# Kernel tuning notes

Measured on AMD Instinct MI355X. Metric: run time of the kernel, lower is better.

Reference implementation:

```python
import jax, jax.numpy as jnp
import numpy as np

B, N, NV = 2, 4096, 32768
HID = 128
XD, YD, ZD = 128, 128, 16  # dense occupancy grid dims (original derives from coord maxima)


def setup_inputs() -> dict:
    key = jax.random.key(0)
    ks = jax.random.split(key, 12)
    position = jax.random.normal(ks[0], (B, N, 3), jnp.float32) * 20.0
    scale = jax.random.uniform(ks[1], (B, N, 3), jnp.float32)
    rotation = jax.random.normal(ks[2], (B, N, 4), jnp.float32)
    opacity = jax.random.uniform(ks[3], (B, N, 1), jnp.float32)
    # sparse voxel coords: [batch_idx, x, y, z]
    b_idx = jax.random.randint(ks[4], (NV, 1), 0, B)
    xs = jax.random.randint(ks[5], (NV, 1), 0, XD)
    ys = jax.random.randint(ks[6], (NV, 1), 0, YD)
    zs = jax.random.randint(ks[7], (NV, 1), 0, ZD)
    voxel_coords = jnp.concatenate([b_idx, xs, ys, zs], axis=1).astype(jnp.int32)
    # MLP params: Linear(11,128) -> ReLU -> Linear(128,128)
    W1 = jax.random.normal(ks[8], (11, HID), jnp.float32) * (1.0 / np.sqrt(11))
    b1 = jnp.zeros((HID,), jnp.float32)
    W2 = jax.random.normal(ks[9], (HID, HID), jnp.float32) * (1.0 / np.sqrt(HID))
    b2 = jnp.zeros((HID,), jnp.float32)
    return {"position": position, "scale": scale, "rotation": rotation,
            "opacity": opacity, "W1": W1, "b1": b1, "W2": W2, "b2": b2,
            "voxel_coords": voxel_coords}


def reference(position, scale, rotation, opacity, W1, b1, W2, b2, voxel_coords):
    # concat gaussian attributes -> (B, N, 11)
    x = jnp.concatenate([position, scale, rotation, opacity], axis=-1)
    x = jnp.maximum(x @ W1 + b1, 0.0) @ W2 + b2  # (B, N, HID)

    # anchor grid: linspace(-50,50, N^(1/3))^3 -> (N, 3)
    n_side = int(round(N ** (1.0 / 3.0)))
    anchor_pos = jnp.linspace(-50.0, 50.0, n_side)
    grid = jnp.stack(jnp.meshgrid(anchor_pos, anchor_pos, anchor_pos, indexing="ij"), axis=-1)
    anchor_grid = grid.reshape(-1, 3)  # (N, 3)

    batch_ids = voxel_coords[:, 0]
    xyz = voxel_coords[:, 1:].astype(jnp.float32)  # (NV, 3)

    # Euclidean cdist (NV, N) via ||a||^2 + ||b||^2 - 2ab
    d2 = (jnp.sum(xyz * xyz, axis=1, keepdims=True)
          + jnp.sum(anchor_grid * anchor_grid, axis=1)[None, :]
          - 2.0 * (xyz @ anchor_grid.T))
    dist = jnp.sqrt(jnp.maximum(d2, 0.0))
    weight = jax.nn.softmax(-dist, axis=-1)  # (NV, N)

    fused = jnp.einsum("vn,bnd->bvd", weight, x)  # (B, NV, HID)

    # scatter into dense 5D occupancy grid (vectorized over all batches)
    occ = jnp.zeros((B, HID, XD, YD, ZD), jnp.float32)
    vals = fused[batch_ids, jnp.arange(NV)]  # (NV, HID) per-voxel feature from its own batch
    occ = occ.at[batch_ids, :, voxel_coords[:, 1], voxel_coords[:, 2], voxel_coords[:, 3]].set(vals)
    return occ
```

## Files before the change

### kernel.cpp

```cpp
#include <hip/hip_runtime.h>
#include <hip/hip_bf16.h>

#define B_    2
#define N_    4096
#define NV_   32768
#define HID_  128
#define XD_   128
#define YD_   128
#define ZD_   16
#define PLANE (XD_*YD_*ZD_)
#define LOCS  (B_*PLANE)
#define STEP  (100.0f/15.0f)
#define KS    4
#define VBL   160
#define L2E   1.4426950408889634f

typedef __attribute__((ext_vector_type(8)))  short short8;
typedef __attribute__((ext_vector_type(16))) float f32x16;
typedef __attribute__((ext_vector_type(4)))  float fv4;

__device__ __forceinline__ float anchor_s(int i) {
    return fmaf((float)i, STEP * L2E, -50.0f * L2E);
}
__device__ __forceinline__ float fexp2(float x) {
    float r; asm("v_exp_f32 %0, %1" : "=v"(r) : "v"(x)); return r;
}
__device__ __forceinline__ unsigned short f2bf(float x) {
    unsigned u = __float_as_uint(x);
    return (unsigned short)((u + 0x7fffu + ((u >> 16) & 1u)) >> 16);
}
__device__ __forceinline__ void gload16(const void* g, void* l) {
    __builtin_amdgcn_global_load_lds(
        (const __attribute__((address_space(1))) unsigned int*)g,
        (__attribute__((address_space(3))) unsigned int*)l, 16, 0, 0);
}

__global__ __launch_bounds__(256) void mlp_kernel(
    const float* __restrict__ pos, const float* __restrict__ scl,
    const float* __restrict__ rot, const float* __restrict__ opa,
    const float* __restrict__ W1,  const float* __restrict__ b1,
    const float* __restrict__ W2,  const float* __restrict__ b2,
    unsigned short* __restrict__ xwT)
{
    int tid = threadIdx.x;
    int j  = tid & 127;
    int rg = tid >> 7;
    int r0 = blockIdx.x * 8;
    __shared__ float sin_[8][11];
    __shared__ float h[8][HID_];
    if (tid < 88) {
        int rr = tid / 11, c = tid - rr*11;
        int r = r0 + rr;
        float val;
        if (c < 3)       val = pos[r*3 + c];
        else if (c < 6)  val = scl[r*3 + (c-3)];
        else if (c < 10) val = rot[r*4 + (c-6)];
        else             val = opa[r];
        sin_[rr][c] = val;
    }
    __syncthreads();
    float bb1 = b1[j];
    #pragma unroll
    for (int q = 0; q < 4; ++q) {
        int rr = rg*4 + q;
        float a = bb1;
        #pragma unroll
        for (int i = 0; i < 11; ++i) a = fmaf(sin_[rr][i], W1[i*HID_ + j], a);
        h[rr][j] = fmaxf(a, 0.0f);
    }
    __syncthreads();
    float bb2 = b2[j];
    float o0 = bb2, o1 = bb2, o2 = bb2, o3 = bb2;
    #pragma unroll 4
    for (int k = 0; k < HID_; ++k) {
        float w2 = W2[k*HID_ + j];
        int rb = rg*4;
        o0 = fmaf(h[rb+0][k], w2, o0);
        o1 = fmaf(h[rb+1][k], w2, o1);
        o2 = fmaf(h[rb+2][k], w2, o2);
        o3 = fmaf(h[rb+3][k], w2, o3);
    }
    float o[4] = {o0, o1, o2, o3};
    #pragma unroll
    for (int q = 0; q < 4; ++q) {
        int r = r0 + rg*4 + q;
        int b = r >> 12, n = r & 4095;
        xwT[((size_t)(b*HID_ + j))*N_ + n] = f2bf(o[q]);
    }
}

__global__ __launch_bounds__(256) void ml_kernel(
    const int* __restrict__ vc, float2* __restrict__ ml,
    int* __restrict__ map, int* __restrict__ cnt, int* __restrict__ vlist)
{
    int gid = blockIdx.x * 256 + threadIdx.x;
    int v = gid >> 3, sub = gid & 7;
    int4 c = ((const int4*)vc)[v];

    if (sub == 0) {
        int loc = ((c.x*XD_ + c.y)*YD_ + c.z)*ZD_ + c.w;
        atomicMax(&map[loc], v);
        int lane = threadIdx.x & 63;
        unsigned long long act = __ballot(1);
        unsigned long long m1 = __ballot(c.x != 0);
        unsigned long long mymask = c.x ? m1 : (act & ~m1);
        int leader = (int)__ffsll(mymask) - 1;
        int total  = __popcll(mymask);
        int rank   = __popcll(mymask & ((1ull << lane) - 1ull));
        int base = 0;
        if (lane == leader) base = atomicAdd(&cnt[c.x], total);
        base = __shfl(base, leader);
        vlist[c.x*NV_ + base + rank] = v;
    }

    float vx = (float)c.y * L2E, vy = (float)c.z * L2E, vz = (float)c.w * L2E;
    float dz2_[16];
    float mindz2 = 1e30f;
    #pragma unroll 16
    for (int iz = 0; iz < 16; ++iz) {
        float t = vz - anchor_s(iz); dz2_[iz] = t*t;
        mindz2 = fminf(mindz2, dz2_[iz]);
    }
    float dxa = vx - anchor_s(sub*2), dxb = vx - anchor_s(sub*2 + 1);
    float dx2_[2] = {dxa*dxa, dxb*dxb};

    float md[4] = {1e30f, 1e30f, 1e30f, 1e30f};
    #pragma unroll
    for (int i = 0; i < 2; ++i) {
        for (int iy = 0; iy < 16; ++iy) {
            float dy = vy - anchor_s(iy);
            float bxy = fmaf(dy, dy, dx2_[i]);
            #pragma unroll 16
            for (int iz = 0; iz < 16; ++iz)
                md[iz & 3] = fminf(md[iz & 3], bxy + dz2_[iz]);
        }
    }
    float m2v = fminf(fminf(md[0], md[1]), fminf(md[2], md[3]));
    #pragma unroll
    for (int off = 1; off < 8; off <<= 1) m2v = fminf(m2v, __shfl_xor(m2v, off));
    float m = sqrtf(m2v);

    float lim = m + 34.0f;
    float lim2 = lim * lim;
    float la = 0.f, lb = 0.f;
    #pragma unroll
    for (int i = 0; i < 2; ++i) {
        for (int iy = 0; iy < 16; ++iy) {
            float dy = vy - anchor_s(iy);
            float bxy = fmaf(dy, dy, dx2_[i]);
            if (bxy + mindz2 <= lim2) {
                #pragma unroll 8
                for (int iz = 0; iz < 16; iz += 2) {
                    la += fexp2(m - sqrtf(bxy + dz2_[iz]));
                    lb += fexp2(m - sqrtf(bxy + dz2_[iz+1]));
                }
            }
        }
    }
    float l = la + lb;
    #pragma unroll
    for (int off = 1; off < 8; off <<= 1) l += __shfl_xor(l, off);
    if (sub == 0) ml[v] = make_float2(m, 1.0f / l);
}

__global__ __launch_bounds__(256) void fuse_kernel(
    const unsigned short* __restrict__ xwT, const float2* __restrict__ ml,
    const int* __restrict__ vc,   const int* __restrict__ vlist,
    const int* __restrict__ cnt,  float* __restrict__ fused_p)
{
    int bid  = blockIdx.x;
    int ks_  = bid & (KS-1);
    int rest = bid >> 2;
    int seg  = (rest >= VBL) ? 1 : 0;
    int bi   = rest - seg*VBL;
    int count = cnt[seg];
    int vbase = bi * 128;
    if (vbase >= count) return;
    int nv = min(128, count - vbase);
    int k0 = ks_ * (N_/KS);

    __shared__ __align__(16) unsigned char sXT[2][16384];
    __shared__ int svid[128];

    int tid = threadIdx.x;
    int w  = tid >> 6, l = tid & 63;
    int h  = l >> 5;
    int cl = l & 31;

    if (tid < 128) svid[tid] = (tid < nv) ? vlist[seg*NV_ + vbase + tid] : -1;

    int vloc = w*32 + cl;
    float pml = -1e30f, pvx = 0.f, pvy = 0.f;
    float dz2_[16];
    #pragma unroll 16
    for (int iz = 0; iz < 16; ++iz) dz2_[iz] = 0.f;
    if (vloc < nv) {
        int vid = vlist[seg*NV_ + vbase + vloc];
        int4 c = ((const int4*)vc)[vid];
        pvx = (float)c.y * L2E; pvy = (float)c.z * L2E;
        float pvz = (float)c.w * L2E;
        pml = ml[vid].x;
        #pragma unroll 16
        for (int iz = 0; iz < 16; ++iz) { float t = pvz - anchor_s(iz); dz2_[iz] = t*t; }
    }

    int d0s  = w*32 + (l >> 3);
    int blkX = (l & 7) ^ ((l >> 3) & 7);
    const unsigned short* sb = xwT + (size_t)(seg*128 + d0s)*N_ + blkX*8 + k0;

    auto stage = [&](int bsel, int t) {
        char* ldsb = (char*)&sXT[bsel][0] + w*4096;
        #pragma unroll
        for (int i = 0; i < 4; ++i)
            gload16(sb + (size_t)i*8*N_ + t*64, ldsb + i*1024);
    };

    f32x16 acc[4];
    #pragma unroll
    for (int i = 0; i < 4; ++i) acc[i] = (f32x16)(0.f);

    const int TILES = (N_/KS)/64;
    stage(0, 0);

    for (int t = 0; t < TILES; ++t) {
        int cur = t & 1;
        unsigned pk_[4][4];
        int nb = k0 + t*64;
        #pragma unroll
        for (int kss = 0; kss < 4; ++kss) {
            int kg = nb + kss*16;
            float ax = anchor_s(kg >> 8);
            float ay = anchor_s((kg >> 4) & 15);
            float dx = pvx - ax, dy = pvy - ay;
            float bxy = fmaf(dx, dx, dy*dy);
            #pragma unroll
            for (int jj = 0; jj < 4; ++jj) {
                float dA = sqrtf(bxy + dz2_[h*8 + 2*jj]);
                float dB = sqrtf(bxy + dz2_[h*8 + 2*jj + 1]);
                float p0 = fexp2(pml - dA);
                float p1 = fexp2(pml - dB);
                asm("v_cvt_pk_bf16_f32 %0, %1, %2" : "=v"(pk_[kss][jj]) : "v"(p0), "v"(p1));
            }
        }
        __syncthreads();
        if (t + 1 < TILES) stage(cur ^ 1, t + 1);
        #pragma unroll
        for (int kss = 0; kss < 4; ++kss) {
            union { uint4 q; short8 s; } u8;
            u8.q = make_uint4(pk_[kss][0], pk_[kss][1], pk_[kss][2], pk_[kss][3]);
            short8 af = u8.s;
            #pragma unroll
            for (int df = 0; df < 4; ++df) {
                int row = df*32 + cl;
                int blk = (kss*2 + h) ^ (row & 7);
                short8 bf = *(const short8*)&sXT[cur][row*128 + blk*16];
                acc[df] = __builtin_amdgcn_mfma_f32_32x32x16_bf16(af, bf, acc[df], 0, 0, 0);
            }
        }
    }

    float* fp = fused_p + (size_t)ks_ * NV_ * HID_;
    #pragma unroll
    for (int df = 0; df < 4; ++df) {
        int dcol = df*32 + cl;
        #pragma unroll
        for (int reg = 0; reg < 16; ++reg) {
            int vrow = w*32 + (reg & 3) + 8*(reg >> 2) + 4*h;
            int sv = svid[vrow];
            if (sv >= 0)
                __builtin_nontemporal_store(acc[df][reg], &fp[(size_t)sv*HID_ + dcol]);
        }
    }
}

__global__ __launch_bounds__(256) void reduce_kernel(
    const float* __restrict__ fused_p, const float2* __restrict__ ml,
    float* __restrict__ fused)
{
    int idx = blockIdx.x * 256 + threadIdx.x;
    int v = idx >> 5;
    float il = ml[v].y;
    const size_t stride = (size_t)NV_ * HID_ / 4;
    const fv4* p = (const fv4*)fused_p + idx;
    fv4 a = __builtin_nontemporal_load(&p[0]);
    fv4 b = __builtin_nontemporal_load(&p[stride]);
    fv4 c = __builtin_nontemporal_load(&p[2*stride]);
    fv4 d = __builtin_nontemporal_load(&p[3*stride]);
    fv4 o = (a + b + c + d) * il;
    ((fv4*)fused)[idx] = o;
}

__global__ __launch_bounds__(256) void out_kernel(
    const int* __restrict__ map, const float* __restrict__ fused,
    float* __restrict__ out)
{
    int q = blockIdx.x * 256 + threadIdx.x;
    int loc0 = q << 2;
    int b   = loc0 >> 18;
    int rem = loc0 & (PLANE - 1);
    int4 vv = ((const int4*)map)[q];
    const fv4* r0 = (const fv4*)(fused + (size_t)(vv.x < 0 ? 0 : vv.x) * HID_);
    const fv4* r1 = (const fv4*)(fused + (size_t)(vv.y < 0 ? 0 : vv.y) * HID_);
    const fv4* r2 = (const fv4*)(fused + (size_t)(vv.z < 0 ? 0 : vv.z) * HID_);
    const fv4* r3 = (const fv4*)(fused + (size_t)(vv.w < 0 ? 0 : vv.w) * HID_);
    size_t obase = ((size_t)b * HID_) * PLANE + rem;
    const fv4 z4 = (fv4)(0.f);
    #pragma unroll 4
    for (int chb = 0; chb < 32; ++chb) {
        fv4 a = (vv.x >= 0) ? r0[chb] : z4;
        fv4 c = (vv.y >= 0) ? r1[chb] : z4;
        fv4 d = (vv.z >= 0) ? r2[chb] : z4;
        fv4 e = (vv.w >= 0) ? r3[chb] : z4;
        fv4 o0 = {a.x, c.x, d.x, e.x};
        fv4 o1 = {a.y, c.y, d.y, e.y};
        fv4 o2 = {a.z, c.z, d.z, e.z};
        fv4 o3 = {a.w, c.w, d.w, e.w};
        __builtin_nontemporal_store(o0, (fv4*)&out[obase + (size_t)(chb*4 + 0) * PLANE]);
        __builtin_nontemporal_store(o1, (fv4*)&out[obase + (size_t)(chb*4 + 1) * PLANE]);
        __builtin_nontemporal_store(o2, (fv4*)&out[obase + (size_t)(chb*4 + 2) * PLANE]);
        __builtin_nontemporal_store(o3, (fv4*)&out[obase + (size_t)(chb*4 + 3) * PLANE]);
    }
}

extern "C" void kernel_launch(void* const* d_in, const int* in_sizes, int n_in,
                              void* d_out, int out_size, void* d_ws, size_t ws_size,
                              hipStream_t stream) {
    const float* pos = (const float*)d_in[0];
    const float* scl = (const float*)d_in[1];
    const float* rot = (const float*)d_in[2];
    const float* opa = (const float*)d_in[3];
    const float* W1  = (const float*)d_in[4];
    const float* b1  = (const float*)d_in[5];
    const float* W2  = (const float*)d_in[6];
    const float* b2  = (const float*)d_in[7];
    const int*   vc  = (const int*)d_in[8];
    float* out = (float*)d_out;

    char* ws = (char*)d_ws;
    unsigned short* xwT = (unsigned short*)(ws);
    float2* ml      = (float2*)(ws + (2u<<20));
    float*  fused   = (float*) (ws + (4u<<20));
    float*  fused_p = (float*) (ws + (20u<<20));
    int*    map     = (int*)   (ws + (84u<<20));
    int*    vlist   = (int*)   (ws + (86u<<20));
    int*    cnt     = (int*)   (ws + (87u<<20));

    hipMemsetAsync(map, 0xFF, LOCS*sizeof(int), stream);
    hipMemsetAsync(cnt, 0, 2*sizeof(int), stream);

    mlp_kernel<<<(B_*N_)/8, 256, 0, stream>>>(pos, scl, rot, opa, W1, b1, W2, b2, xwT);
    ml_kernel<<<(NV_*8)/256, 256, 0, stream>>>(vc, ml, map, cnt, vlist);
    fuse_kernel<<<2*VBL*KS, 256, 0, stream>>>(xwT, ml, vc, vlist, cnt, fused_p);
    reduce_kernel<<<(NV_*HID_/4)/256, 256, 0, stream>>>(fused_p, ml, fused);
    out_kernel<<<LOCS/(256*4), 256, 0, stream>>>(map, fused, out);
}
```

Measured before the change: 317.2 us.

## Overlap output zero-fill with fuse GEMM and fold split-K reduce into scatter

The fuse kernel grid is interleaved with extra blocks that write zeros to output locations whose group of four cells holds no voxel, so the bulk of the memory-bound zero fill runs alongside the compute-bound GEMM blocks. The separate reduce kernel is removed. The output kernel now handles only groups that contain a voxel, summing the four split-K partials and scaling by the softmax normaliser directly. This saves one launch and one full round trip of the fused intermediate, at the cost of zero blocks competing with GEMM blocks for bandwidth and more scattered partial reads in the output kernel.

```diff
diff --git a/kernel.cpp b/kernel.cpp
--- a/kernel.cpp
+++ b/kernel.cpp
@@ -13,6 +13,8 @@
 #define STEP  (100.0f/15.0f)
 #define KS    4
 #define VBL   160
+#define NFUSE (2*VBL*KS)
+#define NZERO 512
 #define L2E   1.4426950408889634f
 
 typedef __attribute__((ext_vector_type(8)))  short short8;
@@ -163,14 +165,38 @@
     if (sub == 0) ml[v] = make_float2(m, 1.0f / l);
 }
 
-__global__ __launch_bounds__(256) void fuse_kernel(
+__global__ __launch_bounds__(256) void fusezero_kernel(
     const unsigned short* __restrict__ xwT, const float2* __restrict__ ml,
     const int* __restrict__ vc,   const int* __restrict__ vlist,
-    const int* __restrict__ cnt,  float* __restrict__ fused_p)
+    const int* __restrict__ cnt,  float* __restrict__ fused_p,
+    const int* __restrict__ map,  float* __restrict__ out)
 {
-    int bid  = blockIdx.x;
-    int ks_  = bid & (KS-1);
-    int rest = bid >> 2;
+    int bid = blockIdx.x;
+    int g = bid / 7, r = bid - g*7;
+    int tid = threadIdx.x;
+
+    if (r == 3 || r == 6) {
+        int zidx = g*2 + (r == 6 ? 1 : 0);
+        int q = zidx*256 + tid;
+        int4 vv = ((const int4*)map)[q];
+        if ((vv.x & vv.y & vv.z & vv.w) < 0) {
+            int loc0 = q << 2;
+            int b   = loc0 >> 18;
+            int rem = loc0 & (PLANE - 1);
+            size_t obase = ((size_t)b * HID_) * PLANE + rem;
+            const fv4 z4 = (fv4)(0.f);
+            #pragma unroll 4
+            for (int ch = 0; ch < HID_; ++ch)
+                __builtin_nontemporal_store(z4, (fv4*)&out[obase + (size_t)ch * PLANE]);
+        }
+        return;
+    }
+
+    const int fcnt_[7] = {0, 1, 2, 3, 3, 4, 5};
+    int item = g*5 + fcnt_[r];
+
+    int ks_  = item & (KS-1);
+    int rest = item >> 2;
     int seg  = (rest >= VBL) ? 1 : 0;
     int bi   = rest - seg*VBL;
     int count = cnt[seg];
@@ -182,7 +208,6 @@
     __shared__ __align__(16) unsigned char sXT[2][16384];
     __shared__ int svid[128];
 
-    int tid = threadIdx.x;
     int w  = tid >> 6, l = tid & 63;
     int h  = l >> 5;
     int cl = l & 31;
@@ -191,37 +216,35 @@
 
     int vloc = w*32 + cl;
     float pml = -1e30f, pvx = 0.f, pvy = 0.f;
-    float dz2_[16];
-    #pragma unroll 16
-    for (int iz = 0; iz < 16; ++iz) dz2_[iz] = 0.f;
+    float dz2h[8];
+    #pragma unroll
+    for (int z = 0; z < 8; ++z) dz2h[z] = 0.f;
     if (vloc < nv) {
         int vid = vlist[seg*NV_ + vbase + vloc];
-        int4 c = ((const int4*)vc)[vid];
-        pvx = (float)c.y * L2E; pvy = (float)c.z * L2E;
-        float pvz = (float)c.w * L2E;
+        int4 cc = ((const int4*)vc)[vid];
+        pvx = (float)cc.y * L2E; pvy = (float)cc.z * L2E;
+        float pvz = (float)cc.w * L2E;
         pml = ml[vid].x;
-        #pragma unroll 16
-        for (int iz = 0; iz < 16; ++iz) { float t = pvz - anchor_s(iz); dz2_[iz] = t*t; }
+        #pragma unroll
+        for (int z = 0; z < 8; ++z) { float t0 = pvz - anchor_s(h*8 + z); dz2h[z] = t0*t0; }
     }
 
     int d0s  = w*32 + (l >> 3);
     int blkX = (l & 7) ^ ((l >> 3) & 7);
-    const unsigned short* sb = xwT + (size_t)(seg*128 + d0s)*N_ + blkX*8 + k0;
-
-    auto stage = [&](int bsel, int t) {
-        char* ldsb = (char*)&sXT[bsel][0] + w*4096;
+    const unsigned short* sb = xwT + (size_t)(seg*HID_ + d0s)*N_ + blkX*8 + k0;
+
+    f32x16 acc[4];
+    #pragma unroll
+    for (int i = 0; i < 4; ++i) acc[i] = (f32x16)(0.f);
+
+    {
+        char* ldsb = (char*)&sXT[0][0] + w*4096;
         #pragma unroll
         for (int i = 0; i < 4; ++i)
-            gload16(sb + (size_t)i*8*N_ + t*64, ldsb + i*1024);
-    };
-
-    f32x16 acc[4];
-    #pragma unroll
-    for (int i = 0; i < 4; ++i) acc[i] = (f32x16)(0.f);
+            gload16(sb + (size_t)i*8*N_, ldsb + i*1024);
+    }
 
     const int TILES = (N_/KS)/64;
-    stage(0, 0);
-
     for (int t = 0; t < TILES; ++t) {
         int cur = t & 1;
         unsigned pk_[4][4];
@@ -235,15 +258,20 @@
             float bxy = fmaf(dx, dx, dy*dy);
             #pragma unroll
             for (int jj = 0; jj < 4; ++jj) {
-                float dA = sqrtf(bxy + dz2_[h*8 + 2*jj]);
-                float dB = sqrtf(bxy + dz2_[h*8 + 2*jj + 1]);
+                float dA = sqrtf(bxy + dz2h[2*jj]);
+                float dB = sqrtf(bxy + dz2h[2*jj + 1]);
                 float p0 = fexp2(pml - dA);
                 float p1 = fexp2(pml - dB);
                 asm("v_cvt_pk_bf16_f32 %0, %1, %2" : "=v"(pk_[kss][jj]) : "v"(p0), "v"(p1));
             }
         }
         __syncthreads();
-        if (t + 1 < TILES) stage(cur ^ 1, t + 1);
+        if (t + 1 < TILES) {
+            char* ldsb = (char*)&sXT[cur^1][0] + w*4096;
+            #pragma unroll
+            for (int i = 0; i < 4; ++i)
+                gload16(sb + (size_t)i*8*N_ + (t+1)*64, ldsb + i*1024);
+        }
         #pragma unroll
         for (int kss = 0; kss < 4; ++kss) {
             union { uint4 q; short8 s; } u8;
@@ -267,54 +295,53 @@
         for (int reg = 0; reg < 16; ++reg) {
             int vrow = w*32 + (reg & 3) + 8*(reg >> 2) + 4*h;
             int sv = svid[vrow];
-            if (sv >= 0)
-                __builtin_nontemporal_store(acc[df][reg], &fp[(size_t)sv*HID_ + dcol]);
-        }
-    }
-}
-
-__global__ __launch_bounds__(256) void reduce_kernel(
-    const float* __restrict__ fused_p, const float2* __restrict__ ml,
-    float* __restrict__ fused)
-{
-    int idx = blockIdx.x * 256 + threadIdx.x;
-    int v = idx >> 5;
-    float il = ml[v].y;
-    const size_t stride = (size_t)NV_ * HID_ / 4;
-    const fv4* p = (const fv4*)fused_p + idx;
-    fv4 a = __builtin_nontemporal_load(&p[0]);
-    fv4 b = __builtin_nontemporal_load(&p[stride]);
-    fv4 c = __builtin_nontemporal_load(&p[2*stride]);
-    fv4 d = __builtin_nontemporal_load(&p[3*stride]);
-    fv4 o = (a + b + c + d) * il;
-    ((fv4*)fused)[idx] = o;
-}
-
-__global__ __launch_bounds__(256) void out_kernel(
-    const int* __restrict__ map, const float* __restrict__ fused,
-    float* __restrict__ out)
+            if (sv >= 0) fp[(size_t)sv*HID_ + dcol] = acc[df][reg];
+        }
+    }
+}
+
+__global__ __launch_bounds__(256) void outv_kernel(
+    const int* __restrict__ map, const float* __restrict__ fused_p,
+    const float2* __restrict__ ml, float* __restrict__ out)
 {
     int q = blockIdx.x * 256 + threadIdx.x;
+    int4 vv = ((const int4*)map)[q];
+    if ((vv.x & vv.y & vv.z & vv.w) < 0) return;
+
     int loc0 = q << 2;
     int b   = loc0 >> 18;
     int rem = loc0 & (PLANE - 1);
-    int4 vv = ((const int4*)map)[q];
-    const fv4* r0 = (const fv4*)(fused + (size_t)(vv.x < 0 ? 0 : vv.x) * HID_);
-    const fv4* r1 = (const fv4*)(fused + (size_t)(vv.y < 0 ? 0 : vv.y) * HID_);
-    const fv4* r2 = (const fv4*)(fused + (size_t)(vv.z < 0 ? 0 : vv.z) * HID_);
-    const fv4* r3 = (const fv4*)(fused + (size_t)(vv.w < 0 ? 0 : vv.w) * HID_);
     size_t obase = ((size_t)b * HID_) * PLANE + rem;
-    const fv4 z4 = (fv4)(0.f);
-    #pragma unroll 4
+    const size_t S4 = (size_t)NV_ * HID_ / 4;
+    const fv4* P = (const fv4*)fused_p;
+
+    int   va[4] = {vv.x, vv.y, vv.z, vv.w};
+    float il[4];
+    const fv4* rp[4];
+    #pragma unroll
+    for (int k = 0; k < 4; ++k) {
+        il[k] = (va[k] >= 0) ? ml[va[k]].y : 0.0f;
+        rp[k] = P + (size_t)(va[k] >= 0 ? va[k] : 0) * 32;
+    }
+
     for (int chb = 0; chb < 32; ++chb) {
-        fv4 a = (vv.x >= 0) ? r0[chb] : z4;
-        fv4 c = (vv.y >= 0) ? r1[chb] : z4;
-        fv4 d = (vv.z >= 0) ? r2[chb] : z4;
-        fv4 e = (vv.w >= 0) ? r3[chb] : z4;
-        fv4 o0 = {a.x, c.x, d.x, e.x};
-        fv4 o1 = {a.y, c.y, d.y, e.y};
-        fv4 o2 = {a.z, c.z, d.z, e.z};
-        fv4 o3 = {a.w, c.w, d.w, e.w};
+        fv4 vals[4];
+        #pragma unroll
+        for (int k = 0; k < 4; ++k) {
+            fv4 s = (fv4)(0.f);
+            if (va[k] >= 0) {
+                fv4 a = rp[k][chb];
+                fv4 bq = rp[k][chb + S4];
+                fv4 cq = rp[k][chb + 2*S4];
+                fv4 dq = rp[k][chb + 3*S4];
+                s = (a + bq + cq + dq) * il[k];
+            }
+            vals[k] = s;
+        }
+        fv4 o0 = {vals[0].x, vals[1].x, vals[2].x, vals[3].x};
+        fv4 o1 = {vals[0].y, vals[1].y, vals[2].y, vals[3].y};
+        fv4 o2 = {vals[0].z, vals[1].z, vals[2].z, vals[3].z};
+        fv4 o3 = {vals[0].w, vals[1].w, vals[2].w, vals[3].w};
         __builtin_nontemporal_store(o0, (fv4*)&out[obase + (size_t)(chb*4 + 0) * PLANE]);
         __builtin_nontemporal_store(o1, (fv4*)&out[obase + (size_t)(chb*4 + 1) * PLANE]);
         __builtin_nontemporal_store(o2, (fv4*)&out[obase + (size_t)(chb*4 + 2) * PLANE]);
@@ -339,18 +366,17 @@
     char* ws = (char*)d_ws;
     unsigned short* xwT = (unsigned short*)(ws);
     float2* ml      = (float2*)(ws + (2u<<20));
-    float*  fused   = (float*) (ws + (4u<<20));
-    float*  fused_p = (float*) (ws + (20u<<20));
-    int*    map     = (int*)   (ws + (84u<<20));
-    int*    vlist   = (int*)   (ws + (86u<<20));
-    int*    cnt     = (int*)   (ws + (87u<<20));
+    float*  fused_p = (float*) (ws + (4u<<20));
+    int*    map     = (int*)   (ws + (68u<<20));
+    int*    vlist   = (int*)   (ws + (70u<<20));
+    int*    cnt     = (int*)   (ws + (71u<<20));
 
     hipMemsetAsync(map, 0xFF, LOCS*sizeof(int), stream);
     hipMemsetAsync(cnt, 0, 2*sizeof(int), stream);
 
     mlp_kernel<<<(B_*N_)/8, 256, 0, stream>>>(pos, scl, rot, opa, W1, b1, W2, b2, xwT);
     ml_kernel<<<(NV_*8)/256, 256, 0, stream>>>(vc, ml, map, cnt, vlist);
-    fuse_kernel<<<2*VBL*KS, 256, 0, stream>>>(xwT, ml, vc, vlist, cnt, fused_p);
-    reduce_kernel<<<(NV_*HID_/4)/256, 256, 0, stream>>>(fused_p, ml, fused);
-    out_kernel<<<LOCS/(256*4), 256, 0, stream>>>(map, fused, out);
-}
+    fusezero_kernel<<<NFUSE + NZERO, 256, 0, stream>>>(xwT, ml, vc, vlist, cnt,
+                                                       fused_p, map, out);
+    outv_kernel<<<LOCS/(256*4), 256, 0, stream>>>(map, fused_p, ml, out);
+}
```

New measurement: 388.8 us. 22.6% more time.

## Split output write into zero-fill of empty quads and compacted occupied-quad scatter

Applied to the files above, without the earlier changes.

Adds a compaction kernel that builds a list of output quads (four consecutive z-locations) holding at least one voxel, and a zero kernel that writes all-zero channels for empty quads before the fuse step. The final output kernel now loops only over the compacted occupied quads with a fixed grid of 128 blocks, instead of visiting every grid location after the reduction. This moves most of the dense zero-writing off the tail of the dependency chain, but adds two extra launches, an atomic counter, and a small persistent grid that may underuse bandwidth for the occupied scatter. The fuse kernel also keeps only the 8 per-half dz² values it needs in registers instead of all 16, and inlines the staging lambda.

```diff
diff --git a/kernel.cpp b/kernel.cpp
--- a/kernel.cpp
+++ b/kernel.cpp
@@ -10,9 +10,11 @@
 #define ZD_   16
 #define PLANE (XD_*YD_*ZD_)
 #define LOCS  (B_*PLANE)
+#define NQ    (LOCS/4)
 #define STEP  (100.0f/15.0f)
 #define KS    4
 #define VBL   160
+#define NFUSE (2*VBL*KS)
 #define L2E   1.4426950408889634f
 
 typedef __attribute__((ext_vector_type(8)))  short short8;
@@ -163,6 +165,41 @@
     if (sub == 0) ml[v] = make_float2(m, 1.0f / l);
 }
 
+__global__ __launch_bounds__(256) void qcompact_kernel(
+    const int* __restrict__ map, int* __restrict__ qlist, int* __restrict__ qcount)
+{
+    int q = blockIdx.x * 256 + threadIdx.x;
+    int4 vv = ((const int4*)map)[q];
+    bool valid = !((vv.x & vv.y & vv.z & vv.w) < 0);
+    int lane = threadIdx.x & 63;
+    unsigned long long mk = __ballot(valid);
+    if (valid) {
+        int leader = (int)__ffsll(mk) - 1;
+        int rank = __popcll(mk & ((1ull << lane) - 1ull));
+        int base = 0;
+        if (lane == leader) base = atomicAdd(qcount, __popcll(mk));
+        base = __shfl(base, leader);
+        qlist[base + rank] = q;
+    }
+}
+
+__global__ __launch_bounds__(256) void zero_kernel(
+    const int* __restrict__ map, float* __restrict__ out)
+{
+    int q = blockIdx.x * 256 + threadIdx.x;
+    int4 vv = ((const int4*)map)[q];
+    if ((vv.x & vv.y & vv.z & vv.w) < 0) {
+        int loc0 = q << 2;
+        int b   = loc0 >> 18;
+        int rem = loc0 & (PLANE - 1);
+        size_t obase = ((size_t)b * HID_) * PLANE + rem;
+        const fv4 z4 = (fv4)(0.f);
+        #pragma unroll 4
+        for (int ch = 0; ch < HID_; ++ch)
+            __builtin_nontemporal_store(z4, (fv4*)&out[obase + (size_t)ch * PLANE]);
+    }
+}
+
 __global__ __launch_bounds__(256) void fuse_kernel(
     const unsigned short* __restrict__ xwT, const float2* __restrict__ ml,
     const int* __restrict__ vc,   const int* __restrict__ vlist,
@@ -191,37 +228,35 @@
 
     int vloc = w*32 + cl;
     float pml = -1e30f, pvx = 0.f, pvy = 0.f;
-    float dz2_[16];
-    #pragma unroll 16
-    for (int iz = 0; iz < 16; ++iz) dz2_[iz] = 0.f;
+    float dz2h[8];
+    #pragma unroll
+    for (int z = 0; z < 8; ++z) dz2h[z] = 0.f;
     if (vloc < nv) {
         int vid = vlist[seg*NV_ + vbase + vloc];
-        int4 c = ((const int4*)vc)[vid];
-        pvx = (float)c.y * L2E; pvy = (float)c.z * L2E;
-        float pvz = (float)c.w * L2E;
+        int4 cc = ((const int4*)vc)[vid];
+        pvx = (float)cc.y * L2E; pvy = (float)cc.z * L2E;
+        float pvz = (float)cc.w * L2E;
         pml = ml[vid].x;
-        #pragma unroll 16
-        for (int iz = 0; iz < 16; ++iz) { float t = pvz - anchor_s(iz); dz2_[iz] = t*t; }
+        #pragma unroll
+        for (int z = 0; z < 8; ++z) { float t0 = pvz - anchor_s(h*8 + z); dz2h[z] = t0*t0; }
     }
 
     int d0s  = w*32 + (l >> 3);
     int blkX = (l & 7) ^ ((l >> 3) & 7);
-    const unsigned short* sb = xwT + (size_t)(seg*128 + d0s)*N_ + blkX*8 + k0;
-
-    auto stage = [&](int bsel, int t) {
-        char* ldsb = (char*)&sXT[bsel][0] + w*4096;
+    const unsigned short* sb = xwT + (size_t)(seg*HID_ + d0s)*N_ + blkX*8 + k0;
+
+    f32x16 acc[4];
+    #pragma unroll
+    for (int i = 0; i < 4; ++i) acc[i] = (f32x16)(0.f);
+
+    {
+        char* ldsb = (char*)&sXT[0][0] + w*4096;
         #pragma unroll
         for (int i = 0; i < 4; ++i)
-            gload16(sb + (size_t)i*8*N_ + t*64, ldsb + i*1024);
-    };
-
-    f32x16 acc[4];
-    #pragma unroll
-    for (int i = 0; i < 4; ++i) acc[i] = (f32x16)(0.f);
+            gload16(sb + (size_t)i*8*N_, ldsb + i*1024);
+    }
 
     const int TILES = (N_/KS)/64;
-    stage(0, 0);
-
     for (int t = 0; t < TILES; ++t) {
         int cur = t & 1;
         unsigned pk_[4][4];
@@ -235,15 +270,20 @@
             float bxy = fmaf(dx, dx, dy*dy);
             #pragma unroll
             for (int jj = 0; jj < 4; ++jj) {
-                float dA = sqrtf(bxy + dz2_[h*8 + 2*jj]);
-                float dB = sqrtf(bxy + dz2_[h*8 + 2*jj + 1]);
+                float dA = sqrtf(bxy + dz2h[2*jj]);
+                float dB = sqrtf(bxy + dz2h[2*jj + 1]);
                 float p0 = fexp2(pml - dA);
                 float p1 = fexp2(pml - dB);
                 asm("v_cvt_pk_bf16_f32 %0, %1, %2" : "=v"(pk_[kss][jj]) : "v"(p0), "v"(p1));
             }
         }
         __syncthreads();
-        if (t + 1 < TILES) stage(cur ^ 1, t + 1);
+        if (t + 1 < TILES) {
+            char* ldsb = (char*)&sXT[cur^1][0] + w*4096;
+            #pragma unroll
+            for (int i = 0; i < 4; ++i)
+                gload16(sb + (size_t)i*8*N_ + (t+1)*64, ldsb + i*1024);
+        }
         #pragma unroll
         for (int kss = 0; kss < 4; ++kss) {
             union { uint4 q; short8 s; } u8;
@@ -290,35 +330,39 @@
     ((fv4*)fused)[idx] = o;
 }
 
-__global__ __launch_bounds__(256) void out_kernel(
+__global__ __launch_bounds__(256) void outv_kernel(
+    const int* __restrict__ qlist, const int* __restrict__ qcount,
     const int* __restrict__ map, const float* __restrict__ fused,
     float* __restrict__ out)
 {
-    int q = blockIdx.x * 256 + threadIdx.x;
-    int loc0 = q << 2;
-    int b   = loc0 >> 18;
-    int rem = loc0 & (PLANE - 1);
-    int4 vv = ((const int4*)map)[q];
-    const fv4* r0 = (const fv4*)(fused + (size_t)(vv.x < 0 ? 0 : vv.x) * HID_);
-    const fv4* r1 = (const fv4*)(fused + (size_t)(vv.y < 0 ? 0 : vv.y) * HID_);
-    const fv4* r2 = (const fv4*)(fused + (size_t)(vv.z < 0 ? 0 : vv.z) * HID_);
-    const fv4* r3 = (const fv4*)(fused + (size_t)(vv.w < 0 ? 0 : vv.w) * HID_);
-    size_t obase = ((size_t)b * HID_) * PLANE + rem;
-    const fv4 z4 = (fv4)(0.f);
-    #pragma unroll 4
-    for (int chb = 0; chb < 32; ++chb) {
-        fv4 a = (vv.x >= 0) ? r0[chb] : z4;
-        fv4 c = (vv.y >= 0) ? r1[chb] : z4;
-        fv4 d = (vv.z >= 0) ? r2[chb] : z4;
-        fv4 e = (vv.w >= 0) ? r3[chb] : z4;
-        fv4 o0 = {a.x, c.x, d.x, e.x};
-        fv4 o1 = {a.y, c.y, d.y, e.y};
-        fv4 o2 = {a.z, c.z, d.z, e.z};
-        fv4 o3 = {a.w, c.w, d.w, e.w};
-        __builtin_nontemporal_store(o0, (fv4*)&out[obase + (size_t)(chb*4 + 0) * PLANE]);
-        __builtin_nontemporal_store(o1, (fv4*)&out[obase + (size_t)(chb*4 + 1) * PLANE]);
-        __builtin_nontemporal_store(o2, (fv4*)&out[obase + (size_t)(chb*4 + 2) * PLANE]);
-        __builtin_nontemporal_store(o3, (fv4*)&out[obase + (size_t)(chb*4 + 3) * PLANE]);
+    int n = *qcount;
+    for (int i = blockIdx.x*256 + threadIdx.x; i < n; i += 128*256) {
+        int q = qlist[i];
+        int4 vv = ((const int4*)map)[q];
+        int loc0 = q << 2;
+        int b   = loc0 >> 18;
+        int rem = loc0 & (PLANE - 1);
+        size_t obase = ((size_t)b * HID_) * PLANE + rem;
+        const fv4* r0 = (const fv4*)(fused + (size_t)(vv.x < 0 ? 0 : vv.x) * HID_);
+        const fv4* r1 = (const fv4*)(fused + (size_t)(vv.y < 0 ? 0 : vv.y) * HID_);
+        const fv4* r2 = (const fv4*)(fused + (size_t)(vv.z < 0 ? 0 : vv.z) * HID_);
+        const fv4* r3 = (const fv4*)(fused + (size_t)(vv.w < 0 ? 0 : vv.w) * HID_);
+        const fv4 z4 = (fv4)(0.f);
+        #pragma unroll 4
+        for (int chb = 0; chb < 32; ++chb) {
+            fv4 a = (vv.x >= 0) ? r0[chb] : z4;
+            fv4 c = (vv.y >= 0) ? r1[chb] : z4;
+            fv4 d = (vv.z >= 0) ? r2[chb] : z4;
+            fv4 e = (vv.w >= 0) ? r3[chb] : z4;
+            fv4 o0 = {a.x, c.x, d.x, e.x};
+            fv4 o1 = {a.y, c.y, d.y, e.y};
+            fv4 o2 = {a.z, c.z, d.z, e.z};
+            fv4 o3 = {a.w, c.w, d.w, e.w};
+            __builtin_nontemporal_store(o0, (fv4*)&out[obase + (size_t)(chb*4 + 0) * PLANE]);
+            __builtin_nontemporal_store(o1, (fv4*)&out[obase + (size_t)(chb*4 + 1) * PLANE]);
+            __builtin_nontemporal_store(o2, (fv4*)&out[obase + (size_t)(chb*4 + 2) * PLANE]);
+            __builtin_nontemporal_store(o3, (fv4*)&out[obase + (size_t)(chb*4 + 3) * PLANE]);
+        }
     }
 }
 
@@ -344,13 +388,16 @@
     int*    map     = (int*)   (ws + (84u<<20));
     int*    vlist   = (int*)   (ws + (86u<<20));
     int*    cnt     = (int*)   (ws + (87u<<20));
+    int*    qlist   = (int*)   (ws + (88u<<20));
 
     hipMemsetAsync(map, 0xFF, LOCS*sizeof(int), stream);
-    hipMemsetAsync(cnt, 0, 2*sizeof(int), stream);
+    hipMemsetAsync(cnt, 0, 3*sizeof(int), stream);
 
     mlp_kernel<<<(B_*N_)/8, 256, 0, stream>>>(pos, scl, rot, opa, W1, b1, W2, b2, xwT);
     ml_kernel<<<(NV_*8)/256, 256, 0, stream>>>(vc, ml, map, cnt, vlist);
-    fuse_kernel<<<2*VBL*KS, 256, 0, stream>>>(xwT, ml, vc, vlist, cnt, fused_p);
+    qcompact_kernel<<<NQ/256, 256, 0, stream>>>(map, qlist, cnt + 2);
+    zero_kernel<<<NQ/256, 256, 0, stream>>>(map, out);
+    fuse_kernel<<<NFUSE, 256, 0, stream>>>(xwT, ml, vc, vlist, cnt, fused_p);
     reduce_kernel<<<(NV_*HID_/4)/256, 256, 0, stream>>>(fused_p, ml, fused);
-    out_kernel<<<LOCS/(256*4), 256, 0, stream>>>(map, fused, out);
-}
+    outv_kernel<<<128, 256, 0, stream>>>(qlist, cnt + 2, map, fused, out);
+}
```

After: 479.4 us. +51.1%, slower.
